# Kernel tuning notes

Measured on AMD Instinct MI355X. Metric: run time of the kernel, lower is better.

## Reference

```python
import jax, jax.numpy as jnp
import numpy as np

B = 524288        # batch
W = 64            # window_size


def setup_inputs() -> dict:
    key = jax.random.key(0)
    k1, k2, k3 = jax.random.split(key, 3)
    x = jax.random.normal(k1, (B, W), dtype=jnp.float32)
    theta = 0.01 * jax.random.normal(k2, (W, 2), dtype=jnp.float32)
    w = jax.random.normal(k3, (1, 1), dtype=jnp.float32)
    b = jnp.zeros((1,), dtype=jnp.float32)
    return {"x": x, "theta": theta, "w": w, "b": b}


def _expval_z(x, theta):
    """Single-qubit re-uploading circuit: for each t, RX(x_t) RY(th_t0) RZ(th_t1)
    applied to |0>, then <Z>. State carried as two complex amplitudes [B]."""
    bsz = x.shape[0]
    s0 = jnp.ones((bsz,), dtype=jnp.complex64)
    s1 = jnp.zeros((bsz,), dtype=jnp.complex64)

    def step(state, inp):
        s0, s1 = state
        xt, th = inp                      # xt: [B], th: [2]
        # RX(xt): [[c, -i s], [-i s, c]], half-angle
        c = jnp.cos(0.5 * xt).astype(jnp.complex64)
        s = jnp.sin(0.5 * xt).astype(jnp.complex64)
        n0 = c * s0 - 1j * s * s1
        n1 = -1j * s * s0 + c * s1
        # RY(th[0]): [[cy, -sy], [sy, cy]]
        cy = jnp.cos(0.5 * th[0]).astype(jnp.complex64)
        sy = jnp.sin(0.5 * th[0]).astype(jnp.complex64)
        m0 = cy * n0 - sy * n1
        m1 = sy * n0 + cy * n1
        # RZ(th[1]): diag(e^{-i th/2}, e^{+i th/2})
        p = jnp.exp(-0.5j * th[1].astype(jnp.complex64))
        return (p * m0, jnp.conj(p) * m1), None

    (s0, s1), _ = jax.lax.scan(step, (s0, s1), (x.T, theta))  # xs leading dim W
    # <Z> = |s0|^2 - |s1|^2 (real)
    return ((s0 * jnp.conj(s0) - s1 * jnp.conj(s1)).real).astype(jnp.float32)


def reference(x, theta, w, b):
    z = _expval_z(x, theta)               # [B]
    return z * w[0, 0] + b[0]             # Linear(1,1) readout, squeezed -> [B]
```

## Files before the change

kernel.cpp:

```cpp
#include <hip/hip_runtime.h>

#define WSZ    64
#define BLOCK  256
#define INV2PI 0.15915494309189535f

#define VM_WAIT4 asm volatile("s_waitcnt vmcnt(4)" ::: "memory")
#define VM_WAIT0 asm volatile("s_waitcnt vmcnt(0)" ::: "memory")

__device__ __forceinline__ float rl(float v, int t) {
    return __builtin_bit_cast(float, __builtin_amdgcn_readlane(__builtin_bit_cast(int, v), t));
}

__global__ __launch_bounds__(BLOCK) void sq_main(
    const float* __restrict__ x,
    const float* __restrict__ theta,
    const float* __restrict__ w,
    const float* __restrict__ bias,
    float* __restrict__ out)
{
    __shared__ float4 xs4[4][2][256];

    const int tid  = threadIdx.x;
    const int lane = tid & 63;
    const int wid  = tid >> 6;
    const size_t wrow0 = (size_t)blockIdx.x * BLOCK + wid * 64;
    const float* xw = x + wrow0 * WSZ;

    float4* buf0 = &xs4[wid][0][0];
    float4* buf1 = &xs4[wid][1][0];

    float2 th = reinterpret_cast<const float2*>(theta)[lane];
    float sa = __builtin_amdgcn_sinf(th.x * INV2PI);
    float ca = __builtin_amdgcn_cosf(th.x * INV2PI);
    float sb = __builtin_amdgcn_sinf(th.y * INV2PI);
    float cb = __builtin_amdgcn_cosf(th.y * INV2PI);
    float m00 = cb * ca, m01 = -sb,     m02 = cb * sa;
    float m10 = sb * ca, m11 = cb,      m12 = sb * sa;
    float m20 = -sa,     m22 = ca;

    auto issue = [&](int q, float4* buf) {
        #pragma unroll
        for (int i = 0; i < 4; ++i) {
            int l    = i * 64 + lane;
            int row  = l >> 2;
            int cl   = l & 3;
            int cg   = cl ^ ((row >> 1) & 3);
            const float* src = xw + (size_t)row * WSZ + q * 16 + cg * 4;
            __builtin_amdgcn_global_load_lds(
                (const __attribute__((address_space(1))) void*)src,
                (__attribute__((address_space(3))) void*)&buf[i * 64], 16, 0, 0);
        }
    };

    float vx = 0.0f, vy = 0.0f, vz = 1.0f;
    const int key = (lane >> 1) & 3;

    auto quarter = [&](int q, const float4* buf) {
        #pragma unroll
        for (int c = 0; c < 4; ++c) {
            float4 xv = buf[lane * 4 + (c ^ key)];
            float xr[4] = {xv.x, xv.y, xv.z, xv.w};
            #pragma unroll
            for (int j = 0; j < 4; ++j) {
                const int t = q * 16 + c * 4 + j;
                float r  = xr[j] * INV2PI;
                float s  = __builtin_amdgcn_sinf(r);
                float co = __builtin_amdgcn_cosf(r);
                float y1 = co * vy - s * vz;
                float z1 = s  * vy + co * vz;
                float nx = rl(m00,t) * vx + rl(m01,t) * y1 + rl(m02,t) * z1;
                float ny = rl(m10,t) * vx + rl(m11,t) * y1 + rl(m12,t) * z1;
                float nz = rl(m20,t) * vx + rl(m22,t) * z1;
                vx = nx; vy = ny; vz = nz;
            }
        }
    };

    issue(0, buf0);
    issue(1, buf1);
    VM_WAIT4;
    quarter(0, buf0);
    issue(2, buf0);
    VM_WAIT4;
    quarter(1, buf1);
    issue(3, buf1);
    VM_WAIT4;
    quarter(2, buf0);
    VM_WAIT0;
    quarter(3, buf1);

    out[wrow0 + lane] = vz * w[0] + bias[0];
}

extern "C" void kernel_launch(void* const* d_in, const int* in_sizes, int n_in,
                              void* d_out, int out_size, void* d_ws, size_t ws_size,
                              hipStream_t stream) {
    const float* x     = (const float*)d_in[0];
    const float* theta = (const float*)d_in[1];
    const float* w     = (const float*)d_in[2];
    const float* b     = (const float*)d_in[3];
    float* out = (float*)d_out;

    int nrows = out_size;
    int grid  = nrows / BLOCK;
    sq_main<<<grid, BLOCK, 0, stream>>>(x, theta, w, b, out);
}
```

Before: 42.00 us.

## Replace async global-to-LDS loads with register-staged prefetch into padded LDS

Drops the direct global_load_lds double-buffered pipeline with its XOR swizzle and explicit vmcnt waits. Each wave now loads float4 chunks into registers, writes them into a per-wave LDS tile padded to a stride of 20 floats to avoid bank conflicts, and prefetches the next column chunk into registers while the current chunk is computed. This makes the copy path simpler and leaves wait placement to the compiler. In exchange it adds VGPR pressure and an extra register-to-LDS write step, and the wave reads and rewrites a single LDS buffer with no barrier between them.

```diff
diff --git a/kernel.cpp b/kernel.cpp
--- a/kernel.cpp
+++ b/kernel.cpp
@@ -2,10 +2,8 @@
 
 #define WSZ    64
 #define BLOCK  256
+#define STRIDE 20
 #define INV2PI 0.15915494309189535f
-
-#define VM_WAIT4 asm volatile("s_waitcnt vmcnt(4)" ::: "memory")
-#define VM_WAIT0 asm volatile("s_waitcnt vmcnt(0)" ::: "memory")
 
 __device__ __forceinline__ float rl(float v, int t) {
     return __builtin_bit_cast(float, __builtin_amdgcn_readlane(__builtin_bit_cast(int, v), t));
@@ -18,76 +16,67 @@
     const float* __restrict__ bias,
     float* __restrict__ out)
 {
-    __shared__ float4 xs4[4][2][256];
+    __shared__ float xs[4][WSZ * STRIDE];
 
     const int tid  = threadIdx.x;
     const int lane = tid & 63;
     const int wid  = tid >> 6;
     const size_t wrow0 = (size_t)blockIdx.x * BLOCK + wid * 64;
     const float* xw = x + wrow0 * WSZ;
-
-    float4* buf0 = &xs4[wid][0][0];
-    float4* buf1 = &xs4[wid][1][0];
+    float* ws = xs[wid];
 
     float2 th = reinterpret_cast<const float2*>(theta)[lane];
     float sa = __builtin_amdgcn_sinf(th.x * INV2PI);
     float ca = __builtin_amdgcn_cosf(th.x * INV2PI);
     float sb = __builtin_amdgcn_sinf(th.y * INV2PI);
     float cb = __builtin_amdgcn_cosf(th.y * INV2PI);
-    float m00 = cb * ca, m01 = -sb,     m02 = cb * sa;
-    float m10 = sb * ca, m11 = cb,      m12 = sb * sa;
+    float m00 = cb * ca, m01 = -sb, m02 = cb * sa;
+    float m10 = sb * ca, m11 = cb,  m12 = sb * sa;
     float m20 = -sa,     m22 = ca;
 
-    auto issue = [&](int q, float4* buf) {
-        #pragma unroll
-        for (int i = 0; i < 4; ++i) {
-            int l    = i * 64 + lane;
-            int row  = l >> 2;
-            int cl   = l & 3;
-            int cg   = cl ^ ((row >> 1) & 3);
-            const float* src = xw + (size_t)row * WSZ + q * 16 + cg * 4;
-            __builtin_amdgcn_global_load_lds(
-                (const __attribute__((address_space(1))) void*)src,
-                (__attribute__((address_space(3))) void*)&buf[i * 64], 16, 0, 0);
-        }
-    };
+    const int lrow  = lane >> 2;
+    const int lslot = lane & 3;
+
+    float4 stage[4];
+    #pragma unroll
+    for (int j = 0; j < 4; ++j)
+        stage[j] = *reinterpret_cast<const float4*>(
+            xw + (size_t)(j * 16 + lrow) * WSZ + lslot * 4);
 
     float vx = 0.0f, vy = 0.0f, vz = 1.0f;
-    const int key = (lane >> 1) & 3;
 
-    auto quarter = [&](int q, const float4* buf) {
+    #pragma unroll
+    for (int c = 0; c < 4; ++c) {
         #pragma unroll
-        for (int c = 0; c < 4; ++c) {
-            float4 xv = buf[lane * 4 + (c ^ key)];
+        for (int j = 0; j < 4; ++j)
+            *reinterpret_cast<float4*>(&ws[(j * 16 + lrow) * STRIDE + lslot * 4]) = stage[j];
+
+        if (c < 3) {
+            #pragma unroll
+            for (int j = 0; j < 4; ++j)
+                stage[j] = *reinterpret_cast<const float4*>(
+                    xw + (size_t)(j * 16 + lrow) * WSZ + (c + 1) * 16 + lslot * 4);
+        }
+
+        #pragma unroll
+        for (int c2 = 0; c2 < 4; ++c2) {
+            float4 xv = *reinterpret_cast<const float4*>(&ws[lane * STRIDE + c2 * 4]);
             float xr[4] = {xv.x, xv.y, xv.z, xv.w};
             #pragma unroll
             for (int j = 0; j < 4; ++j) {
-                const int t = q * 16 + c * 4 + j;
+                const int t = c * 16 + c2 * 4 + j;
                 float r  = xr[j] * INV2PI;
                 float s  = __builtin_amdgcn_sinf(r);
                 float co = __builtin_amdgcn_cosf(r);
                 float y1 = co * vy - s * vz;
                 float z1 = s  * vy + co * vz;
-                float nx = rl(m00,t) * vx + rl(m01,t) * y1 + rl(m02,t) * z1;
-                float ny = rl(m10,t) * vx + rl(m11,t) * y1 + rl(m12,t) * z1;
-                float nz = rl(m20,t) * vx + rl(m22,t) * z1;
+                float nx = rl(m00, t) * vx + rl(m01, t) * y1 + rl(m02, t) * z1;
+                float ny = rl(m10, t) * vx + rl(m11, t) * y1 + rl(m12, t) * z1;
+                float nz = rl(m20, t) * vx + rl(m22, t) * z1;
                 vx = nx; vy = ny; vz = nz;
             }
         }
-    };
-
-    issue(0, buf0);
-    issue(1, buf1);
-    VM_WAIT4;
-    quarter(0, buf0);
-    issue(2, buf0);
-    VM_WAIT4;
-    quarter(1, buf1);
-    issue(3, buf1);
-    VM_WAIT4;
-    quarter(2, buf0);
-    VM_WAIT0;
-    quarter(3, buf1);
+    }
 
     out[wrow0 + lane] = vz * w[0] + bias[0];
 }
```

Result: no change. 42.29 us (+0.7%).
